# Kernel tuning notes

Hardware: AMD Instinct MI355X
Metric: run time of the kernel (lower is better)

Reference implementation:

```python
import jax, jax.numpy as jnp
import numpy as np

HIDDEN = [256, 256, 256]
COND = 30
NB_STEPS = 20  # Clenshaw-Curtis quadrature order -> NB_STEPS+1 nodes


def cc_weights_steps(nb_steps):
    # Clenshaw-Curtis weights/nodes on [-1, 1] (UMNN compute_cc_weights)
    lam = np.arange(nb_steps + 1, dtype=np.float64).reshape(-1, 1)
    lam = np.cos(lam @ lam.T * np.pi / nb_steps)
    lam[:, 0] *= 0.5
    lam[:, -1] *= 0.5
    lam = lam * 2.0 / nb_steps
    W = np.arange(nb_steps + 1, dtype=np.float64).reshape(-1, 1)
    W[1::2] = 0.0
    W = 2.0 / (1.0 - W ** 2)
    W[0] = 1.0
    W[1::2] = 0.0
    cc_w = (lam.T @ W).flatten()          # [S]
    steps = np.cos(np.arange(nb_steps + 1) * np.pi / nb_steps)  # [S]
    return jnp.asarray(cc_w, jnp.float32), jnp.asarray(steps, jnp.float32)


def mlp(inp, Ws, bs):
    # IntegrandNet: Linear+ReLU chain, final layer ELU(x)+1 (strictly positive)
    y = inp
    n = len(Ws)
    for i in range(n):
        y = y @ Ws[i] + bs[i]
        y = jax.nn.relu(y) if i < n - 1 else jax.nn.elu(y) + 1.0
    return y[..., 0]


def setup_inputs() -> dict:
    key = jax.random.key(0)
    ks = jax.random.split(key, 12)
    B, D = 512, 32
    x = jax.random.normal(ks[0], (B, D), jnp.float32)
    h = jax.random.normal(ks[1], (B, D, COND), jnp.float32)
    dims = [1 + COND] + HIDDEN + [1]
    params = {}
    for i in range(len(dims) - 1):
        params[f"W{i}"] = jax.random.normal(ks[2 + 2 * i], (dims[i], dims[i + 1]), jnp.float32) / np.sqrt(dims[i]).astype(np.float32)
        params[f"b{i}"] = jnp.zeros((dims[i + 1],), jnp.float32)
    return {"x": x, "h": h, **params}


def reference(x, h, W0, b0, W1, b1, W2, b2, W3, b3):
    Ws = [W0, W1, W2, W3]
    bs = [b0, b1, b2, b3]
    B, D = x.shape
    S = NB_STEPS + 1
    cc_w, steps = cc_weights_steps(NB_STEPS)
    # x0 = 0, xT = x -> quadrature nodes X = xT * (steps + 1) / 2, shape [B, S, D]
    X = x[:, None, :] * (steps[None, :, None] + 1.0) * 0.5
    hb = jnp.broadcast_to(h[:, None, :, :], (B, S, D, COND))
    inp = jnp.concatenate([X[..., None], hb], axis=-1)  # [B, S, D, 1+COND]
    f = mlp(inp, Ws, bs)                                 # [B, S, D] positive integrand
    z_est = jnp.einsum('bsd,s->bd', f, cc_w) * x * 0.5   # integral over [0, x]
    z = z_est + h[:, :, 0]                               # add offset z0
    # second output: integrand evaluated at x (the transform's Jacobian diag)
    inp_x = jnp.concatenate([x[..., None], h], axis=-1)  # [B, D, 1+COND]
    jac = mlp(inp_x, Ws, bs)                             # [B, D]
    return z, jac
```

## Files before the change

### kernel.cpp

```cpp
#include <hip/hip_runtime.h>
#include <math.h>

#define NB        512
#define ND        32
#define NCOND     30
#define NS        21
#define NBD       (NB*ND)
#define NROWS     (NBD*NS)
#define MBLK      64
#define NBLOCKS   (NROWS/MBLK)

#define W0P_ELEMS (1*16*64*8)
#define W1P_ELEMS (8*16*64*8)
#define W3P_ELEMS (8*64*8)
#define WP_TOTAL  (W0P_ELEMS + 2*W1P_ELEMS + W3P_ELEMS)

typedef __bf16 bf8 __attribute__((ext_vector_type(8)));
typedef float  fx4 __attribute__((ext_vector_type(4)));
typedef unsigned short us8 __attribute__((ext_vector_type(8)));

__device__ __forceinline__ unsigned short f2bf(float f) {
  unsigned int u = __float_as_uint(f);
  u += 0x7FFFu + ((u >> 16) & 1u);
  return (unsigned short)(u >> 16);
}

__global__ void prep_pack(const float* __restrict__ W0,
                          const float* __restrict__ W1,
                          const float* __restrict__ W2,
                          const float* __restrict__ W3,
                          unsigned short* __restrict__ wp) {
  int t = blockIdx.x * blockDim.x + threadIdx.x;
  if (t >= WP_TOTAL / 8) return;
  int base = t * 8;
  us8 out;
  if (base >= W0P_ELEMS + 2 * W1P_ELEMS) {
    int rem  = base - (W0P_ELEMS + 2 * W1P_ELEMS);
    int lane = (rem >> 3) & 63;
    int ktl  = rem >> 9;
    int k0   = ktl * 32 + (lane >> 4) * 8;
#pragma unroll
    for (int i = 0; i < 8; ++i)
      out[i] = ((lane & 15) == 0) ? f2bf(W3[k0 + i]) : (unsigned short)0;
  } else {
    const float* W; int rem, K;
    if (base < W0P_ELEMS)                  { W = W0; rem = base;                 K = 31;  }
    else if (base < W0P_ELEMS + W1P_ELEMS) { W = W1; rem = base - W0P_ELEMS;     K = 256; }
    else                                   { W = W2; rem = base - W0P_ELEMS - W1P_ELEMS; K = 256; }
    int lane = (rem >> 3) & 63;
    int ct   = (rem >> 9) & 15;
    int ktl  =  rem >> 13;
    int j  = ct * 16 + (lane & 15);
    int k0 = ktl * 32 + (lane >> 4) * 8;
#pragma unroll
    for (int i = 0; i < 8; ++i) {
      int k = k0 + i;
      out[i] = (k < K) ? f2bf(W[k * 256 + j]) : (unsigned short)0;
    }
  }
  *reinterpret_cast<us8*>(wp + base) = out;
}


#define ACC_ZERO                                                                 \
  _Pragma("unroll")                                                              \
  for (int rt = 0; rt < 4; ++rt)                                                 \
    _Pragma("unroll")                                                            \
    for (int ct = 0; ct < 4; ++ct) acc[rt][ct] = fx4{0.f, 0.f, 0.f, 0.f};

#define LOADW4(S0,S1,S2,S3, WB, KT)                                              \
  S0 = *reinterpret_cast<const bf8*>((WB) + (((KT) * 16 + cgrp * 4 + 0) * 64 + lane) * 8); \
  S1 = *reinterpret_cast<const bf8*>((WB) + (((KT) * 16 + cgrp * 4 + 1) * 64 + lane) * 8); \
  S2 = *reinterpret_cast<const bf8*>((WB) + (((KT) * 16 + cgrp * 4 + 2) * 64 + lane) * 8); \
  S3 = *reinterpret_cast<const bf8*>((WB) + (((KT) * 16 + cgrp * 4 + 3) * 64 + lane) * 8);

#define KSTEP(W0_,W1_,W2_,W3_, KT)                                               \
  {                                                                              \
    int m0 =  0 + colb;                                                          \
    int m1 = 16 + colb;                                                          \
    int m2 = 32 + colb;                                                          \
    int m3 = 48 + colb;                                                          \
    bf8 a0 = *reinterpret_cast<const bf8*>(ldsAct + (((unsigned)(m0 * 512 + (KT) * 64 + khalf * 16)) ^ ((unsigned)((m0 & 15) << 4)))); \
    bf8 a1 = *reinterpret_cast<const bf8*>(ldsAct + (((unsigned)(m1 * 512 + (KT) * 64 + khalf * 16)) ^ ((unsigned)((m1 & 15) << 4)))); \
    bf8 a2 = *reinterpret_cast<const bf8*>(ldsAct + (((unsigned)(m2 * 512 + (KT) * 64 + khalf * 16)) ^ ((unsigned)((m2 & 15) << 4)))); \
    bf8 a3 = *reinterpret_cast<const bf8*>(ldsAct + (((unsigned)(m3 * 512 + (KT) * 64 + khalf * 16)) ^ ((unsigned)((m3 & 15) << 4)))); \
    __builtin_amdgcn_s_setprio(1);                                               \
    acc[0][0] = __builtin_amdgcn_mfma_f32_16x16x32_bf16(W0_, a0, acc[0][0], 0, 0, 0); \
    acc[0][1] = __builtin_amdgcn_mfma_f32_16x16x32_bf16(W1_, a0, acc[0][1], 0, 0, 0); \
    acc[0][2] = __builtin_amdgcn_mfma_f32_16x16x32_bf16(W2_, a0, acc[0][2], 0, 0, 0); \
    acc[0][3] = __builtin_amdgcn_mfma_f32_16x16x32_bf16(W3_, a0, acc[0][3], 0, 0, 0); \
    acc[1][0] = __builtin_amdgcn_mfma_f32_16x16x32_bf16(W0_, a1, acc[1][0], 0, 0, 0); \
    acc[1][1] = __builtin_amdgcn_mfma_f32_16x16x32_bf16(W1_, a1, acc[1][1], 0, 0, 0); \
    acc[1][2] = __builtin_amdgcn_mfma_f32_16x16x32_bf16(W2_, a1, acc[1][2], 0, 0, 0); \
    acc[1][3] = __builtin_amdgcn_mfma_f32_16x16x32_bf16(W3_, a1, acc[1][3], 0, 0, 0); \
    acc[2][0] = __builtin_amdgcn_mfma_f32_16x16x32_bf16(W0_, a2, acc[2][0], 0, 0, 0); \
    acc[2][1] = __builtin_amdgcn_mfma_f32_16x16x32_bf16(W1_, a2, acc[2][1], 0, 0, 0); \
    acc[2][2] = __builtin_amdgcn_mfma_f32_16x16x32_bf16(W2_, a2, acc[2][2], 0, 0, 0); \
    acc[2][3] = __builtin_amdgcn_mfma_f32_16x16x32_bf16(W3_, a2, acc[2][3], 0, 0, 0); \
    acc[3][0] = __builtin_amdgcn_mfma_f32_16x16x32_bf16(W0_, a3, acc[3][0], 0, 0, 0); \
    acc[3][1] = __builtin_amdgcn_mfma_f32_16x16x32_bf16(W1_, a3, acc[3][1], 0, 0, 0); \
    acc[3][2] = __builtin_amdgcn_mfma_f32_16x16x32_bf16(W2_, a3, acc[3][2], 0, 0, 0); \
    acc[3][3] = __builtin_amdgcn_mfma_f32_16x16x32_bf16(W3_, a3, acc[3][3], 0, 0, 0); \
    __builtin_amdgcn_s_setprio(0);                                               \
  }

#define DENSE_PIPE(WB, NWB)                                                      \
  KSTEP(wa0,wa1,wa2,wa3, 0) LOADW4(wa0,wa1,wa2,wa3, WB, 2)                       \
  KSTEP(wb0,wb1,wb2,wb3, 1) LOADW4(wb0,wb1,wb2,wb3, WB, 3)                       \
  KSTEP(wa0,wa1,wa2,wa3, 2) LOADW4(wa0,wa1,wa2,wa3, WB, 4)                       \
  KSTEP(wb0,wb1,wb2,wb3, 3) LOADW4(wb0,wb1,wb2,wb3, WB, 5)                       \
  KSTEP(wa0,wa1,wa2,wa3, 4) LOADW4(wa0,wa1,wa2,wa3, WB, 6)                       \
  KSTEP(wb0,wb1,wb2,wb3, 5) LOADW4(wb0,wb1,wb2,wb3, WB, 7)                       \
  KSTEP(wa0,wa1,wa2,wa3, 6) LOADW4(wa0,wa1,wa2,wa3, NWB, 0)                      \
  KSTEP(wb0,wb1,wb2,wb3, 7) LOADW4(wb0,wb1,wb2,wb3, NWB, 1)

#define DENSE_LAST(WB)                                                           \
  KSTEP(wa0,wa1,wa2,wa3, 0) LOADW4(wa0,wa1,wa2,wa3, WB, 2)                       \
  KSTEP(wb0,wb1,wb2,wb3, 1) LOADW4(wb0,wb1,wb2,wb3, WB, 3)                       \
  KSTEP(wa0,wa1,wa2,wa3, 2) LOADW4(wa0,wa1,wa2,wa3, WB, 4)                       \
  KSTEP(wb0,wb1,wb2,wb3, 3) LOADW4(wb0,wb1,wb2,wb3, WB, 5)                       \
  KSTEP(wa0,wa1,wa2,wa3, 4) LOADW4(wa0,wa1,wa2,wa3, WB, 6)                       \
  KSTEP(wb0,wb1,wb2,wb3, 5) LOADW4(wb0,wb1,wb2,wb3, WB, 7)                       \
  KSTEP(wa0,wa1,wa2,wa3, 6)                                                      \
  KSTEP(wb0,wb1,wb2,wb3, 7)

#define ACT_STORE(BIAS)                                                          \
  {                                                                              \
    float4 bv0 = *reinterpret_cast<const float4*>((BIAS) + (cgrp * 4 + 0) * 16 + khalf * 4); \
    float4 bv1 = *reinterpret_cast<const float4*>((BIAS) + (cgrp * 4 + 1) * 16 + khalf * 4); \
    float4 bv2 = *reinterpret_cast<const float4*>((BIAS) + (cgrp * 4 + 2) * 16 + khalf * 4); \
    float4 bv3 = *reinterpret_cast<const float4*>((BIAS) + (cgrp * 4 + 3) * 16 + khalf * 4); \
    _Pragma("unroll")                                                            \
    for (int rt = 0; rt < 4; ++rt) {                                             \
      int m = rt * 16 + colb;                                                    \
      unsigned int sbase = (unsigned int)(m * 512);                              \
      unsigned int swz   = (unsigned int)((m & 15) << 4);                        \
      _Pragma("unroll")                                                          \
      for (int ct = 0; ct < 4; ++ct) {                                           \
        float4 bv = (ct == 0) ? bv0 : (ct == 1) ? bv1 : (ct == 2) ? bv2 : bv3;   \
        int n0 = (cgrp * 4 + ct) * 16 + khalf * 4;                               \
        float v0 = fmaxf(acc[rt][ct][0] + bv.x, 0.f);                            \
        float v1 = fmaxf(acc[rt][ct][1] + bv.y, 0.f);                            \
        float v2 = fmaxf(acc[rt][ct][2] + bv.z, 0.f);                            \
        float v3 = fmaxf(acc[rt][ct][3] + bv.w, 0.f);                            \
        unsigned int p0, p1;                                                     \
        asm("v_cvt_pk_bf16_f32 %0, %1, %2" : "=v"(p0) : "v"(v0), "v"(v1));       \
        asm("v_cvt_pk_bf16_f32 %0, %1, %2" : "=v"(p1) : "v"(v2), "v"(v3));       \
        uint2 pk; pk.x = p0; pk.y = p1;                                          \
        *reinterpret_cast<uint2*>(ldsAct + ((sbase + (unsigned int)(n0 * 2)) ^ swz)) = pk; \
      }                                                                          \
    }                                                                            \
  }

__global__ __launch_bounds__(256, 2)
void mlp_kernel(const float* __restrict__ x, const float* __restrict__ h,
                const float* __restrict__ b0, const float* __restrict__ b1,
                const float* __restrict__ b2, const float* __restrict__ b3,
                const unsigned short* __restrict__ wp,
                float* __restrict__ fbuf) {
  __shared__ __align__(16) unsigned char ldsAct[64 * 512];
  unsigned char* ldsIn = ldsAct;

  int tid  = threadIdx.x;
  int wv   = tid >> 6;
  int lane = tid & 63;
  int cgrp = wv;
  int colb  = lane & 15;
  int khalf = lane >> 4;
  int R0 = blockIdx.x * MBLK;

  const unsigned short* wb1p = wp + W0P_ELEMS;
  const unsigned short* wb2p = wp + W0P_ELEMS + W1P_ELEMS;
  const unsigned short* w3p  = wp + W0P_ELEMS + 2 * W1P_ELEMS;

  bf8 wa0, wa1, wa2, wa3, wb0, wb1, wb2, wb3;
  LOADW4(wa0, wa1, wa2, wa3, wp, 0);

  {
    int r = tid >> 2;
    int q = tid & 3;
    int gr = R0 + r;
    unsigned int bd = (unsigned int)gr / NS;
    int s = gr - (int)bd * NS;
    float xv = x[bd];
    float node = xv * (cosf((float)s * 0.15707963267948966f) + 1.0f) * 0.5f;
    const float* hrow = h + bd * NCOND;
    us8 au;
#pragma unroll
    for (int i = 0; i < 8; ++i) {
      int c = q * 8 + i;
      float v;
      if (c == 0)       v = node;
      else if (c <= 30) v = hrow[c - 1];
      else              v = 0.0f;
      au[i] = f2bf(v);
    }
    unsigned int off = (unsigned int)(r * 64 + q * 16) ^ (unsigned int)((r & 3) << 4);
    *reinterpret_cast<us8*>(ldsIn + off) = au;
  }
  __syncthreads();

  fx4 acc[4][4];

  {
    ACC_ZERO;
#pragma unroll
    for (int rt = 0; rt < 4; ++rt) {
      int m = rt * 16 + colb;
      unsigned int off = (unsigned int)(m * 64 + khalf * 16) ^ (unsigned int)((m & 3) << 4);
      bf8 a = *reinterpret_cast<const bf8*>(ldsIn + off);
      acc[rt][0] = __builtin_amdgcn_mfma_f32_16x16x32_bf16(wa0, a, acc[rt][0], 0, 0, 0);
      acc[rt][1] = __builtin_amdgcn_mfma_f32_16x16x32_bf16(wa1, a, acc[rt][1], 0, 0, 0);
      acc[rt][2] = __builtin_amdgcn_mfma_f32_16x16x32_bf16(wa2, a, acc[rt][2], 0, 0, 0);
      acc[rt][3] = __builtin_amdgcn_mfma_f32_16x16x32_bf16(wa3, a, acc[rt][3], 0, 0, 0);
    }
    LOADW4(wa0, wa1, wa2, wa3, wb1p, 0);
    LOADW4(wb0, wb1, wb2, wb3, wb1p, 1);
    __syncthreads();
    ACT_STORE(b0);
  }
  __syncthreads();

  ACC_ZERO;
  DENSE_PIPE(wb1p, wb2p);
  __syncthreads();
  ACT_STORE(b1);
  __syncthreads();

  ACC_ZERO;
  DENSE_LAST(wb2p);
  __syncthreads();
  ACT_STORE(b2);
  __syncthreads();

  {
    fx4 a3 = fx4{0.f, 0.f, 0.f, 0.f};
    int m = wv * 16 + colb;
    unsigned int abase = (unsigned int)(m * 512 + khalf * 16);
    unsigned int aswz  = (unsigned int)((m & 15) << 4);
#pragma unroll
    for (int kt = 0; kt < 8; ++kt) {
      bf8 w3f = *reinterpret_cast<const bf8*>(w3p + (kt * 64 + lane) * 8);
      bf8 a = *reinterpret_cast<const bf8*>(ldsAct + ((abase + (unsigned)(kt * 64)) ^ aswz));
      a3 = __builtin_amdgcn_mfma_f32_16x16x32_bf16(w3f, a, a3, 0, 0, 0);
    }
    if (lane < 16) {
      float y = a3[0] + b3[0];
      float f = (y > 0.f) ? (y + 1.f) : expf(y);
      fbuf[R0 + wv * 16 + lane] = f;
    }
  }
}

__global__ void reduce_kernel(const float* __restrict__ x, const float* __restrict__ h,
                              const float* __restrict__ fbuf, float* __restrict__ out) {
  __shared__ float ccw[NS];
  int tid = threadIdx.x;
  if (tid < NS) {
    double acc = 0.0;
#pragma unroll
    for (int i = 0; i <= 20; i += 2) {
      double wi = (i == 0) ? 1.0 : 2.0 / (1.0 - (double)(i * i));
      acc += cos((double)(i * tid) * 3.141592653589793 / 20.0) * wi;
    }
    double edge = (tid == 0 || tid == 20) ? 0.5 : 1.0;
    ccw[tid] = (float)(acc * 0.1 * edge);
  }
  __syncthreads();
  int t = blockIdx.x * blockDim.x + tid;
  if (t >= NBD) return;
  const float* fb = fbuf + t * NS;
  float acc = 0.f;
#pragma unroll
  for (int i = 0; i < NS; ++i) acc += fb[i] * ccw[i];
  float z = acc * x[t] * 0.5f + h[t * NCOND];
  out[t] = z;
  out[NBD + t] = fb[0];
}

extern "C" void kernel_launch(void* const* d_in, const int* in_sizes, int n_in,
                              void* d_out, int out_size, void* d_ws, size_t ws_size,
                              hipStream_t stream) {
  (void)in_sizes; (void)n_in; (void)out_size; (void)ws_size;
  const float* x  = (const float*)d_in[0];
  const float* h  = (const float*)d_in[1];
  const float* W0 = (const float*)d_in[2];
  const float* b0 = (const float*)d_in[3];
  const float* W1 = (const float*)d_in[4];
  const float* b1 = (const float*)d_in[5];
  const float* W2 = (const float*)d_in[6];
  const float* b2 = (const float*)d_in[7];
  const float* W3 = (const float*)d_in[8];
  const float* b3 = (const float*)d_in[9];

  unsigned short* wp = (unsigned short*)d_ws;
  float* fbuf = (float*)((char*)d_ws + WP_TOTAL * sizeof(unsigned short));
  float* out  = (float*)d_out;

  prep_pack<<<(WP_TOTAL / 8 + 255) / 256, 256, 0, stream>>>(W0, W1, W2, W3, wp);
  mlp_kernel<<<NBLOCKS, 256, 0, stream>>>(x, h, b0, b1, b2, b3, wp, fbuf);
  reduce_kernel<<<(NBD + 255) / 256, 256, 0, stream>>>(x, h, fbuf, out);
}
```

Measured before the change: 104.1 us.

## Double per-block row tile to 128 rows to reuse weight fragments

Each block now processes 128 rows instead of 64. Every weight fragment loaded into registers feeds twice as many MFMAs, which halves weight global-load traffic per row. The accumulator array doubles to 8x4 fx4 and LDS grows to 64KB, so launch bounds drop to one block per CU and occupancy falls. Input staging and the final layer are extended to cover the larger tile.

```diff
diff --git a/kernel.cpp b/kernel.cpp
--- a/kernel.cpp
+++ b/kernel.cpp
@@ -7,7 +7,7 @@
 #define NS        21
 #define NBD       (NB*ND)
 #define NROWS     (NBD*NS)
-#define MBLK      64
+#define MBLK      128
 #define NBLOCKS   (NROWS/MBLK)
 
 #define W0P_ELEMS (1*16*64*8)
@@ -64,7 +64,7 @@
 
 #define ACC_ZERO                                                                 \
   _Pragma("unroll")                                                              \
-  for (int rt = 0; rt < 4; ++rt)                                                 \
+  for (int rt = 0; rt < 8; ++rt)                                                 \
     _Pragma("unroll")                                                            \
     for (int ct = 0; ct < 4; ++ct) acc[rt][ct] = fx4{0.f, 0.f, 0.f, 0.f};
 
@@ -74,33 +74,33 @@
   S2 = *reinterpret_cast<const bf8*>((WB) + (((KT) * 16 + cgrp * 4 + 2) * 64 + lane) * 8); \
   S3 = *reinterpret_cast<const bf8*>((WB) + (((KT) * 16 + cgrp * 4 + 3) * 64 + lane) * 8);
 
+#define KROWS(RT, A_, W0_,W1_,W2_,W3_)                                           \
+    acc[RT][0] = __builtin_amdgcn_mfma_f32_16x16x32_bf16(W0_, A_, acc[RT][0], 0, 0, 0); \
+    acc[RT][1] = __builtin_amdgcn_mfma_f32_16x16x32_bf16(W1_, A_, acc[RT][1], 0, 0, 0); \
+    acc[RT][2] = __builtin_amdgcn_mfma_f32_16x16x32_bf16(W2_, A_, acc[RT][2], 0, 0, 0); \
+    acc[RT][3] = __builtin_amdgcn_mfma_f32_16x16x32_bf16(W3_, A_, acc[RT][3], 0, 0, 0);
+
+#define AOFF(M, KT) (((unsigned)((M) * 512 + (KT) * 64 + khalf * 16)) ^ ((unsigned)(((M) & 15) << 4)))
+
 #define KSTEP(W0_,W1_,W2_,W3_, KT)                                               \
   {                                                                              \
-    int m0 =  0 + colb;                                                          \
-    int m1 = 16 + colb;                                                          \
-    int m2 = 32 + colb;                                                          \
-    int m3 = 48 + colb;                                                          \
-    bf8 a0 = *reinterpret_cast<const bf8*>(ldsAct + (((unsigned)(m0 * 512 + (KT) * 64 + khalf * 16)) ^ ((unsigned)((m0 & 15) << 4)))); \
-    bf8 a1 = *reinterpret_cast<const bf8*>(ldsAct + (((unsigned)(m1 * 512 + (KT) * 64 + khalf * 16)) ^ ((unsigned)((m1 & 15) << 4)))); \
-    bf8 a2 = *reinterpret_cast<const bf8*>(ldsAct + (((unsigned)(m2 * 512 + (KT) * 64 + khalf * 16)) ^ ((unsigned)((m2 & 15) << 4)))); \
-    bf8 a3 = *reinterpret_cast<const bf8*>(ldsAct + (((unsigned)(m3 * 512 + (KT) * 64 + khalf * 16)) ^ ((unsigned)((m3 & 15) << 4)))); \
+    bf8 a0 = *reinterpret_cast<const bf8*>(ldsAct + AOFF(  0 + colb, KT));       \
+    bf8 a1 = *reinterpret_cast<const bf8*>(ldsAct + AOFF( 16 + colb, KT));       \
+    bf8 a2 = *reinterpret_cast<const bf8*>(ldsAct + AOFF( 32 + colb, KT));       \
+    bf8 a3 = *reinterpret_cast<const bf8*>(ldsAct + AOFF( 48 + colb, KT));       \
+    bf8 a4 = *reinterpret_cast<const bf8*>(ldsAct + AOFF( 64 + colb, KT));       \
+    bf8 a5 = *reinterpret_cast<const bf8*>(ldsAct + AOFF( 80 + colb, KT));       \
+    bf8 a6 = *reinterpret_cast<const bf8*>(ldsAct + AOFF( 96 + colb, KT));       \
+    bf8 a7 = *reinterpret_cast<const bf8*>(ldsAct + AOFF(112 + colb, KT));       \
     __builtin_amdgcn_s_setprio(1);                                               \
-    acc[0][0] = __builtin_amdgcn_mfma_f32_16x16x32_bf16(W0_, a0, acc[0][0], 0, 0, 0); \
-    acc[0][1] = __builtin_amdgcn_mfma_f32_16x16x32_bf16(W1_, a0, acc[0][1], 0, 0, 0); \
-    acc[0][2] = __builtin_amdgcn_mfma_f32_16x16x32_bf16(W2_, a0, acc[0][2], 0, 0, 0); \
-    acc[0][3] = __builtin_amdgcn_mfma_f32_16x16x32_bf16(W3_, a0, acc[0][3], 0, 0, 0); \
-    acc[1][0] = __builtin_amdgcn_mfma_f32_16x16x32_bf16(W0_, a1, acc[1][0], 0, 0, 0); \
-    acc[1][1] = __builtin_amdgcn_mfma_f32_16x16x32_bf16(W1_, a1, acc[1][1], 0, 0, 0); \
-    acc[1][2] = __builtin_amdgcn_mfma_f32_16x16x32_bf16(W2_, a1, acc[1][2], 0, 0, 0); \
-    acc[1][3] = __builtin_amdgcn_mfma_f32_16x16x32_bf16(W3_, a1, acc[1][3], 0, 0, 0); \
-    acc[2][0] = __builtin_amdgcn_mfma_f32_16x16x32_bf16(W0_, a2, acc[2][0], 0, 0, 0); \
-    acc[2][1] = __builtin_amdgcn_mfma_f32_16x16x32_bf16(W1_, a2, acc[2][1], 0, 0, 0); \
-    acc[2][2] = __builtin_amdgcn_mfma_f32_16x16x32_bf16(W2_, a2, acc[2][2], 0, 0, 0); \
-    acc[2][3] = __builtin_amdgcn_mfma_f32_16x16x32_bf16(W3_, a2, acc[2][3], 0, 0, 0); \
-    acc[3][0] = __builtin_amdgcn_mfma_f32_16x16x32_bf16(W0_, a3, acc[3][0], 0, 0, 0); \
-    acc[3][1] = __builtin_amdgcn_mfma_f32_16x16x32_bf16(W1_, a3, acc[3][1], 0, 0, 0); \
-    acc[3][2] = __builtin_amdgcn_mfma_f32_16x16x32_bf16(W2_, a3, acc[3][2], 0, 0, 0); \
-    acc[3][3] = __builtin_amdgcn_mfma_f32_16x16x32_bf16(W3_, a3, acc[3][3], 0, 0, 0); \
+    KROWS(0, a0, W0_,W1_,W2_,W3_)                                                \
+    KROWS(1, a1, W0_,W1_,W2_,W3_)                                                \
+    KROWS(2, a2, W0_,W1_,W2_,W3_)                                                \
+    KROWS(3, a3, W0_,W1_,W2_,W3_)                                                \
+    KROWS(4, a4, W0_,W1_,W2_,W3_)                                                \
+    KROWS(5, a5, W0_,W1_,W2_,W3_)                                                \
+    KROWS(6, a6, W0_,W1_,W2_,W3_)                                                \
+    KROWS(7, a7, W0_,W1_,W2_,W3_)                                                \
     __builtin_amdgcn_s_setprio(0);                                               \
   }
 
@@ -131,7 +131,7 @@
     float4 bv2 = *reinterpret_cast<const float4*>((BIAS) + (cgrp * 4 + 2) * 16 + khalf * 4); \
     float4 bv3 = *reinterpret_cast<const float4*>((BIAS) + (cgrp * 4 + 3) * 16 + khalf * 4); \
     _Pragma("unroll")                                                            \
-    for (int rt = 0; rt < 4; ++rt) {                                             \
+    for (int rt = 0; rt < 8; ++rt) {                                             \
       int m = rt * 16 + colb;                                                    \
       unsigned int sbase = (unsigned int)(m * 512);                              \
       unsigned int swz   = (unsigned int)((m & 15) << 4);                        \
@@ -152,13 +152,13 @@
     }                                                                            \
   }
 
-__global__ __launch_bounds__(256, 2)
+__global__ __launch_bounds__(256, 1)
 void mlp_kernel(const float* __restrict__ x, const float* __restrict__ h,
                 const float* __restrict__ b0, const float* __restrict__ b1,
                 const float* __restrict__ b2, const float* __restrict__ b3,
                 const unsigned short* __restrict__ wp,
                 float* __restrict__ fbuf) {
-  __shared__ __align__(16) unsigned char ldsAct[64 * 512];
+  __shared__ __align__(16) unsigned char ldsAct[128 * 512];
   unsigned char* ldsIn = ldsAct;
 
   int tid  = threadIdx.x;
@@ -176,9 +176,11 @@
   bf8 wa0, wa1, wa2, wa3, wb0, wb1, wb2, wb3;
   LOADW4(wa0, wa1, wa2, wa3, wp, 0);
 
-  {
-    int r = tid >> 2;
-    int q = tid & 3;
+#pragma unroll
+  for (int it = 0; it < 2; ++it) {
+    int idx = tid + it * 256;
+    int r = idx >> 2;
+    int q = idx & 3;
     int gr = R0 + r;
     unsigned int bd = (unsigned int)gr / NS;
     int s = gr - (int)bd * NS;
@@ -200,12 +202,12 @@
   }
   __syncthreads();
 
-  fx4 acc[4][4];
+  fx4 acc[8][4];
 
   {
     ACC_ZERO;
 #pragma unroll
-    for (int rt = 0; rt < 4; ++rt) {
+    for (int rt = 0; rt < 8; ++rt) {
       int m = rt * 16 + colb;
       unsigned int off = (unsigned int)(m * 64 + khalf * 16) ^ (unsigned int)((m & 3) << 4);
       bf8 a = *reinterpret_cast<const bf8*>(ldsIn + off);
@@ -234,20 +236,24 @@
   __syncthreads();
 
   {
-    fx4 a3 = fx4{0.f, 0.f, 0.f, 0.f};
-    int m = wv * 16 + colb;
-    unsigned int abase = (unsigned int)(m * 512 + khalf * 16);
-    unsigned int aswz  = (unsigned int)((m & 15) << 4);
+    fx4 a30 = fx4{0.f, 0.f, 0.f, 0.f};
+    fx4 a31 = fx4{0.f, 0.f, 0.f, 0.f};
+    int m0 = wv * 32 + colb;
+    int m1 = wv * 32 + 16 + colb;
 #pragma unroll
     for (int kt = 0; kt < 8; ++kt) {
       bf8 w3f = *reinterpret_cast<const bf8*>(w3p + (kt * 64 + lane) * 8);
-      bf8 a = *reinterpret_cast<const bf8*>(ldsAct + ((abase + (unsigned)(kt * 64)) ^ aswz));
-      a3 = __builtin_amdgcn_mfma_f32_16x16x32_bf16(w3f, a, a3, 0, 0, 0);
+      bf8 a0 = *reinterpret_cast<const bf8*>(ldsAct + AOFF(m0, kt));
+      bf8 a1 = *reinterpret_cast<const bf8*>(ldsAct + AOFF(m1, kt));
+      a30 = __builtin_amdgcn_mfma_f32_16x16x32_bf16(w3f, a0, a30, 0, 0, 0);
+      a31 = __builtin_amdgcn_mfma_f32_16x16x32_bf16(w3f, a1, a31, 0, 0, 0);
     }
     if (lane < 16) {
-      float y = a3[0] + b3[0];
-      float f = (y > 0.f) ? (y + 1.f) : expf(y);
-      fbuf[R0 + wv * 16 + lane] = f;
+      float bias3 = b3[0];
+      float y0 = a30[0] + bias3;
+      float y1 = a31[0] + bias3;
+      fbuf[R0 + wv * 32 + lane]      = (y0 > 0.f) ? (y0 + 1.f) : expf(y0);
+      fbuf[R0 + wv * 32 + 16 + lane] = (y1 > 0.f) ? (y1 + 1.f) : expf(y1);
     }
   }
 }
```

Result: slower. 130.4 us (+25.3%).

## Ping-pong activation LDS buffers to halve barriers and fold bias into accumulator init

Applied to the files above, without the earlier changes.

The single LDS activation buffer becomes two buffers used alternately between layers. Each layer can then write its output straight after its MFMAs, without a barrier to wait for other waves to finish reading, which removes about half of the __syncthreads calls. Bias is now loaded into the accumulators at init instead of being added in the store epilogue. LDS per block doubles to 64 KB, which may limit how many blocks fit on a CU alongside the 2-block launch bound.

```diff
diff --git a/kernel.cpp b/kernel.cpp
--- a/kernel.cpp
+++ b/kernel.cpp
@@ -62,11 +62,20 @@
 }
 
 
-#define ACC_ZERO                                                                 \
-  _Pragma("unroll")                                                              \
-  for (int rt = 0; rt < 4; ++rt)                                                 \
+#define ACC_BIAS(BIAS)                                                           \
+  {                                                                              \
+    float4 bq0 = *reinterpret_cast<const float4*>((BIAS) + (cgrp * 4 + 0) * 16 + khalf * 4); \
+    float4 bq1 = *reinterpret_cast<const float4*>((BIAS) + (cgrp * 4 + 1) * 16 + khalf * 4); \
+    float4 bq2 = *reinterpret_cast<const float4*>((BIAS) + (cgrp * 4 + 2) * 16 + khalf * 4); \
+    float4 bq3 = *reinterpret_cast<const float4*>((BIAS) + (cgrp * 4 + 3) * 16 + khalf * 4); \
     _Pragma("unroll")                                                            \
-    for (int ct = 0; ct < 4; ++ct) acc[rt][ct] = fx4{0.f, 0.f, 0.f, 0.f};
+    for (int rt = 0; rt < 4; ++rt) {                                             \
+      acc[rt][0] = fx4{bq0.x, bq0.y, bq0.z, bq0.w};                              \
+      acc[rt][1] = fx4{bq1.x, bq1.y, bq1.z, bq1.w};                              \
+      acc[rt][2] = fx4{bq2.x, bq2.y, bq2.z, bq2.w};                              \
+      acc[rt][3] = fx4{bq3.x, bq3.y, bq3.z, bq3.w};                              \
+    }                                                                            \
+  }
 
 #define LOADW4(S0,S1,S2,S3, WB, KT)                                              \
   S0 = *reinterpret_cast<const bf8*>((WB) + (((KT) * 16 + cgrp * 4 + 0) * 64 + lane) * 8); \
@@ -74,16 +83,14 @@
   S2 = *reinterpret_cast<const bf8*>((WB) + (((KT) * 16 + cgrp * 4 + 2) * 64 + lane) * 8); \
   S3 = *reinterpret_cast<const bf8*>((WB) + (((KT) * 16 + cgrp * 4 + 3) * 64 + lane) * 8);
 
-#define KSTEP(W0_,W1_,W2_,W3_, KT)                                               \
+#define AOFF(M, KT) (((unsigned)((M) * 512 + (KT) * 64 + khalf * 16)) ^ ((unsigned)(((M) & 15) << 4)))
+
+#define KSTEP(SRC, W0_,W1_,W2_,W3_, KT)                                          \
   {                                                                              \
-    int m0 =  0 + colb;                                                          \
-    int m1 = 16 + colb;                                                          \
-    int m2 = 32 + colb;                                                          \
-    int m3 = 48 + colb;                                                          \
-    bf8 a0 = *reinterpret_cast<const bf8*>(ldsAct + (((unsigned)(m0 * 512 + (KT) * 64 + khalf * 16)) ^ ((unsigned)((m0 & 15) << 4)))); \
-    bf8 a1 = *reinterpret_cast<const bf8*>(ldsAct + (((unsigned)(m1 * 512 + (KT) * 64 + khalf * 16)) ^ ((unsigned)((m1 & 15) << 4)))); \
-    bf8 a2 = *reinterpret_cast<const bf8*>(ldsAct + (((unsigned)(m2 * 512 + (KT) * 64 + khalf * 16)) ^ ((unsigned)((m2 & 15) << 4)))); \
-    bf8 a3 = *reinterpret_cast<const bf8*>(ldsAct + (((unsigned)(m3 * 512 + (KT) * 64 + khalf * 16)) ^ ((unsigned)((m3 & 15) << 4)))); \
+    bf8 a0 = *reinterpret_cast<const bf8*>((SRC) + AOFF( 0 + colb, KT));         \
+    bf8 a1 = *reinterpret_cast<const bf8*>((SRC) + AOFF(16 + colb, KT));         \
+    bf8 a2 = *reinterpret_cast<const bf8*>((SRC) + AOFF(32 + colb, KT));         \
+    bf8 a3 = *reinterpret_cast<const bf8*>((SRC) + AOFF(48 + colb, KT));         \
     __builtin_amdgcn_s_setprio(1);                                               \
     acc[0][0] = __builtin_amdgcn_mfma_f32_16x16x32_bf16(W0_, a0, acc[0][0], 0, 0, 0); \
     acc[0][1] = __builtin_amdgcn_mfma_f32_16x16x32_bf16(W1_, a0, acc[0][1], 0, 0, 0); \
@@ -104,32 +111,28 @@
     __builtin_amdgcn_s_setprio(0);                                               \
   }
 
-#define DENSE_PIPE(WB, NWB)                                                      \
-  KSTEP(wa0,wa1,wa2,wa3, 0) LOADW4(wa0,wa1,wa2,wa3, WB, 2)                       \
-  KSTEP(wb0,wb1,wb2,wb3, 1) LOADW4(wb0,wb1,wb2,wb3, WB, 3)                       \
-  KSTEP(wa0,wa1,wa2,wa3, 2) LOADW4(wa0,wa1,wa2,wa3, WB, 4)                       \
-  KSTEP(wb0,wb1,wb2,wb3, 3) LOADW4(wb0,wb1,wb2,wb3, WB, 5)                       \
-  KSTEP(wa0,wa1,wa2,wa3, 4) LOADW4(wa0,wa1,wa2,wa3, WB, 6)                       \
-  KSTEP(wb0,wb1,wb2,wb3, 5) LOADW4(wb0,wb1,wb2,wb3, WB, 7)                       \
-  KSTEP(wa0,wa1,wa2,wa3, 6) LOADW4(wa0,wa1,wa2,wa3, NWB, 0)                      \
-  KSTEP(wb0,wb1,wb2,wb3, 7) LOADW4(wb0,wb1,wb2,wb3, NWB, 1)
-
-#define DENSE_LAST(WB)                                                           \
-  KSTEP(wa0,wa1,wa2,wa3, 0) LOADW4(wa0,wa1,wa2,wa3, WB, 2)                       \
-  KSTEP(wb0,wb1,wb2,wb3, 1) LOADW4(wb0,wb1,wb2,wb3, WB, 3)                       \
-  KSTEP(wa0,wa1,wa2,wa3, 2) LOADW4(wa0,wa1,wa2,wa3, WB, 4)                       \
-  KSTEP(wb0,wb1,wb2,wb3, 3) LOADW4(wb0,wb1,wb2,wb3, WB, 5)                       \
-  KSTEP(wa0,wa1,wa2,wa3, 4) LOADW4(wa0,wa1,wa2,wa3, WB, 6)                       \
-  KSTEP(wb0,wb1,wb2,wb3, 5) LOADW4(wb0,wb1,wb2,wb3, WB, 7)                       \
-  KSTEP(wa0,wa1,wa2,wa3, 6)                                                      \
-  KSTEP(wb0,wb1,wb2,wb3, 7)
-
-#define ACT_STORE(BIAS)                                                          \
+#define DENSE_PIPE(SRC, WB, NWB)                                                 \
+  KSTEP(SRC, wa0,wa1,wa2,wa3, 0) LOADW4(wa0,wa1,wa2,wa3, WB, 2)                  \
+  KSTEP(SRC, wb0,wb1,wb2,wb3, 1) LOADW4(wb0,wb1,wb2,wb3, WB, 3)                  \
+  KSTEP(SRC, wa0,wa1,wa2,wa3, 2) LOADW4(wa0,wa1,wa2,wa3, WB, 4)                  \
+  KSTEP(SRC, wb0,wb1,wb2,wb3, 3) LOADW4(wb0,wb1,wb2,wb3, WB, 5)                  \
+  KSTEP(SRC, wa0,wa1,wa2,wa3, 4) LOADW4(wa0,wa1,wa2,wa3, WB, 6)                  \
+  KSTEP(SRC, wb0,wb1,wb2,wb3, 5) LOADW4(wb0,wb1,wb2,wb3, WB, 7)                  \
+  KSTEP(SRC, wa0,wa1,wa2,wa3, 6) LOADW4(wa0,wa1,wa2,wa3, NWB, 0)                 \
+  KSTEP(SRC, wb0,wb1,wb2,wb3, 7) LOADW4(wb0,wb1,wb2,wb3, NWB, 1)
+
+#define DENSE_LAST(SRC, WB)                                                      \
+  KSTEP(SRC, wa0,wa1,wa2,wa3, 0) LOADW4(wa0,wa1,wa2,wa3, WB, 2)                  \
+  KSTEP(SRC, wb0,wb1,wb2,wb3, 1) LOADW4(wb0,wb1,wb2,wb3, WB, 3)                  \
+  KSTEP(SRC, wa0,wa1,wa2,wa3, 2) LOADW4(wa0,wa1,wa2,wa3, WB, 4)                  \
+  KSTEP(SRC, wb0,wb1,wb2,wb3, 3) LOADW4(wb0,wb1,wb2,wb3, WB, 5)                  \
+  KSTEP(SRC, wa0,wa1,wa2,wa3, 4) LOADW4(wa0,wa1,wa2,wa3, WB, 6)                  \
+  KSTEP(SRC, wb0,wb1,wb2,wb3, 5) LOADW4(wb0,wb1,wb2,wb3, WB, 7)                  \
+  KSTEP(SRC, wa0,wa1,wa2,wa3, 6)                                                 \
+  KSTEP(SRC, wb0,wb1,wb2,wb3, 7)
+
+#define ACT_STORE(DST)                                                           \
   {                                                                              \
-    float4 bv0 = *reinterpret_cast<const float4*>((BIAS) + (cgrp * 4 + 0) * 16 + khalf * 4); \
-    float4 bv1 = *reinterpret_cast<const float4*>((BIAS) + (cgrp * 4 + 1) * 16 + khalf * 4); \
-    float4 bv2 = *reinterpret_cast<const float4*>((BIAS) + (cgrp * 4 + 2) * 16 + khalf * 4); \
-    float4 bv3 = *reinterpret_cast<const float4*>((BIAS) + (cgrp * 4 + 3) * 16 + khalf * 4); \
     _Pragma("unroll")                                                            \
     for (int rt = 0; rt < 4; ++rt) {                                             \
       int m = rt * 16 + colb;                                                    \
@@ -137,17 +140,16 @@
       unsigned int swz   = (unsigned int)((m & 15) << 4);                        \
       _Pragma("unroll")                                                          \
       for (int ct = 0; ct < 4; ++ct) {                                           \
-        float4 bv = (ct == 0) ? bv0 : (ct == 1) ? bv1 : (ct == 2) ? bv2 : bv3;   \
         int n0 = (cgrp * 4 + ct) * 16 + khalf * 4;                               \
-        float v0 = fmaxf(acc[rt][ct][0] + bv.x, 0.f);                            \
-        float v1 = fmaxf(acc[rt][ct][1] + bv.y, 0.f);                            \
-        float v2 = fmaxf(acc[rt][ct][2] + bv.z, 0.f);                            \
-        float v3 = fmaxf(acc[rt][ct][3] + bv.w, 0.f);                            \
+        float v0 = fmaxf(acc[rt][ct][0], 0.f);                                   \
+        float v1 = fmaxf(acc[rt][ct][1], 0.f);                                   \
+        float v2 = fmaxf(acc[rt][ct][2], 0.f);                                   \
+        float v3 = fmaxf(acc[rt][ct][3], 0.f);                                   \
         unsigned int p0, p1;                                                     \
         asm("v_cvt_pk_bf16_f32 %0, %1, %2" : "=v"(p0) : "v"(v0), "v"(v1));       \
         asm("v_cvt_pk_bf16_f32 %0, %1, %2" : "=v"(p1) : "v"(v2), "v"(v3));       \
         uint2 pk; pk.x = p0; pk.y = p1;                                          \
-        *reinterpret_cast<uint2*>(ldsAct + ((sbase + (unsigned int)(n0 * 2)) ^ swz)) = pk; \
+        *reinterpret_cast<uint2*>((DST) + ((sbase + (unsigned int)(n0 * 2)) ^ swz)) = pk; \
       }                                                                          \
     }                                                                            \
   }
@@ -158,8 +160,9 @@
                 const float* __restrict__ b2, const float* __restrict__ b3,
                 const unsigned short* __restrict__ wp,
                 float* __restrict__ fbuf) {
-  __shared__ __align__(16) unsigned char ldsAct[64 * 512];
-  unsigned char* ldsIn = ldsAct;
+  __shared__ __align__(16) unsigned char ldsA[64 * 512];
+  __shared__ __align__(16) unsigned char ldsB[64 * 512];
+  unsigned char* ldsIn = ldsB;
 
   int tid  = threadIdx.x;
   int wv   = tid >> 6;
@@ -203,7 +206,7 @@
   fx4 acc[4][4];
 
   {
-    ACC_ZERO;
+    ACC_BIAS(b0);
 #pragma unroll
     for (int rt = 0; rt < 4; ++rt) {
       int m = rt * 16 + colb;
@@ -216,21 +219,18 @@
     }
     LOADW4(wa0, wa1, wa2, wa3, wb1p, 0);
     LOADW4(wb0, wb1, wb2, wb3, wb1p, 1);
-    __syncthreads();
-    ACT_STORE(b0);
-  }
-  __syncthreads();
-
-  ACC_ZERO;
-  DENSE_PIPE(wb1p, wb2p);
-  __syncthreads();
-  ACT_STORE(b1);
-  __syncthreads();
-
-  ACC_ZERO;
-  DENSE_LAST(wb2p);
-  __syncthreads();
-  ACT_STORE(b2);
+    ACT_STORE(ldsA);
+  }
+  __syncthreads();
+
+  ACC_BIAS(b1);
+  DENSE_PIPE(ldsA, wb1p, wb2p);
+  ACT_STORE(ldsB);
+  __syncthreads();
+
+  ACC_BIAS(b2);
+  DENSE_LAST(ldsB, wb2p);
+  ACT_STORE(ldsA);
   __syncthreads();
 
   {
@@ -241,7 +241,7 @@
 #pragma unroll
     for (int kt = 0; kt < 8; ++kt) {
       bf8 w3f = *reinterpret_cast<const bf8*>(w3p + (kt * 64 + lane) * 8);
-      bf8 a = *reinterpret_cast<const bf8*>(ldsAct + ((abase + (unsigned)(kt * 64)) ^ aswz));
+      bf8 a = *reinterpret_cast<const bf8*>(ldsA + ((abase + (unsigned)(kt * 64)) ^ aswz));
       a3 = __builtin_amdgcn_mfma_f32_16x16x32_bf16(w3f, a, a3, 0, 0, 0);
     }
     if (lane < 16) {
```

New measurement: 101.5 us. -2.5%, faster.
